# Performance work log

Hardware: AMD Instinct MI355X
Metric: run time of the kernel (lower is better)

Reference implementation:

```python
import jax, jax.numpy as jnp
import numpy as np

HEADS = 4
C = 128            # per-head out channels (hard-coded 128 in the module)
NEG_SLOPE_ATT = 0.2   # GATConv attention leaky_relu slope
NEG_SLOPE = 0.01      # F.leaky_relu default slope


def _diag_output_ids(num_groups, n):
    # ids = base_i + n*j + j for group i, agent j; base_i = i * n^2
    i = np.arange(num_groups)[:, None] * (n * n)
    j = np.arange(n)[None, :] * (n + 1)
    return jnp.asarray((i + j).reshape(-1))


def setup_inputs() -> dict:
    key = jax.random.key(0)
    ks = jax.random.split(key, 12)
    num_groups, n_agents = 12, 48
    N = num_groups * n_agents * n_agents      # 27648 nodes
    E = 442368
    F_in, edge_dim, hidden = 256, 16, 256
    s = 0.05
    return {
        "x": jax.random.normal(ks[0], (N, F_in), jnp.float32),
        "edge_index": jax.random.randint(ks[1], (2, E), 0, N, jnp.int32),
        "edge_attr": jax.random.normal(ks[2], (E, edge_dim), jnp.float32),
        "num_groups": num_groups,
        "agents_per_group": n_agents,
        "W": jax.random.normal(ks[3], (F_in, HEADS * C), jnp.float32) * s,
        "att_src": jax.random.normal(ks[4], (HEADS, C), jnp.float32) * s,
        "att_dst": jax.random.normal(ks[5], (HEADS, C), jnp.float32) * s,
        "W_edge": jax.random.normal(ks[6], (edge_dim, HEADS * C), jnp.float32) * s,
        "att_edge": jax.random.normal(ks[7], (HEADS, C), jnp.float32) * s,
        "bias_gat": jnp.zeros((HEADS * C,), jnp.float32),
        "fc_W": jax.random.normal(ks[8], (HEADS * C, hidden), jnp.float32) * s,
        "fc_b": jnp.zeros((hidden,), jnp.float32),
    }


def _gat_conv(x, src, dst, edge_attr_full, W, att_src, att_dst, W_edge, att_edge, bias):
    N = x.shape[0]
    h = (x @ W).reshape(N, HEADS, C)                       # [N,H,C]
    a_src = jnp.einsum('nhc,hc->nh', h, att_src)           # [N,H]
    a_dst = jnp.einsum('nhc,hc->nh', h, att_dst)
    he = (edge_attr_full @ W_edge).reshape(-1, HEADS, C)   # [E',H,C]
    a_edge = jnp.einsum('ehc,hc->eh', he, att_edge)
    logits = jax.nn.leaky_relu(a_src[src] + a_dst[dst] + a_edge, NEG_SLOPE_ATT)
    # segment softmax over incoming edges of each dst node
    m = jax.ops.segment_max(logits, dst, num_segments=N)   # [N,H]
    e = jnp.exp(logits - m[dst])
    s = jax.ops.segment_sum(e, dst, num_segments=N)
    alpha = e / (s[dst] + 1e-16)                           # [E',H]
    msg = h[src] * alpha[..., None]                        # [E',H,C]
    out = jax.ops.segment_sum(msg, dst, num_segments=N)    # [N,H,C]
    return out.reshape(N, HEADS * C) + bias


def reference(x, edge_index, edge_attr, num_groups, agents_per_group,
              W, att_src, att_dst, W_edge, att_edge, bias_gat, fc_W, fc_b):
    N = x.shape[0]
    # add self-loops (PyG default), self-loop edge_attr = mean fill
    loops = jnp.arange(N, dtype=edge_index.dtype)
    src = jnp.concatenate([edge_index[0], loops])
    dst = jnp.concatenate([edge_index[1], loops])
    ea = jnp.concatenate([edge_attr,
                          jnp.broadcast_to(edge_attr.mean(0), (N, edge_attr.shape[1]))])
    h = jax.nn.leaky_relu(
        _gat_conv(x, src, dst, ea, W, att_src, att_dst, W_edge, att_edge, bias_gat),
        NEG_SLOPE)
    ids = _diag_output_ids(num_groups, agents_per_group)
    # fc_output + leaky_relu then diagonal index-select (select first: same math)
    return jax.nn.leaky_relu(h[ids] @ fc_W + fc_b, NEG_SLOPE)
```

## Files before the change

kernel.cpp:

```cpp
#include <hip/hip_runtime.h>

#define NNODES 27648
#define NEDGES 442368
#define FIN    256
#define HC     512
#define NH     4
#define CDIM   128
#define NAG    48
#define NGRP   12
#define N2     2304
#define NOUT   576
#define CAP    128
#define EDIM   16
#define MPART  512
#define SCANB  (NEDGES/256)
#define ASRCB0 (SCANB + 1)


__device__ __forceinline__ float lrelu(float v, float s){ return v > 0.0f ? v : s * v; }

__device__ __forceinline__ float wsum(float v){
  #pragma unroll
  for (int off = 32; off; off >>= 1) v += __shfl_xor(v, off, 64);
  return v;
}
__device__ __forceinline__ float wmax(float v){
  #pragma unroll
  for (int off = 32; off; off >>= 1) v = fmaxf(v, __shfl_xor(v, off, 64));
  return v;
}

__global__ __launch_bounds__(256) void k_pre(
    const float* __restrict__ W, const float* __restrict__ att_src,
    const float* __restrict__ att_dst, const float* __restrict__ W_edge,
    const float* __restrict__ att_edge, const float* __restrict__ ea,
    float* __restrict__ ws_, float* __restrict__ wd_, float* __restrict__ we_,
    int* __restrict__ counts, float4* __restrict__ easum_part){
  int b = blockIdx.x;
  int tid = threadIdx.x;
  if (b < 11) {
    int g = b * 256 + tid;
    if (g < 1024) {
      int f = g >> 2, h = g & 3;
      const float4* wp = (const float4*)(W + f*HC + h*CDIM);
      const float4* ap = (const float4*)(att_src + h*CDIM);
      float s = 0.f;
      #pragma unroll 8
      for (int c4 = 0; c4 < CDIM/4; c4++){
        float4 wv = wp[c4], av = ap[c4];
        s += wv.x*av.x + wv.y*av.y + wv.z*av.z + wv.w*av.w;
      }
      ws_[g] = s;
    } else if (g < 2048) {
      int gg = g - 1024; int f = gg >> 2, h = gg & 3;
      const float4* wp = (const float4*)(W + f*HC + h*CDIM);
      const float4* ap = (const float4*)(att_dst + h*CDIM);
      float s = 0.f;
      #pragma unroll 8
      for (int c4 = 0; c4 < CDIM/4; c4++){
        float4 wv = wp[c4], av = ap[c4];
        s += wv.x*av.x + wv.y*av.y + wv.z*av.z + wv.w*av.w;
      }
      wd_[gg] = s;
    } else if (g < 2112) {
      int gg = g - 2048; int d = gg >> 2, h = gg & 3;
      const float4* wp = (const float4*)(W_edge + d*HC + h*CDIM);
      const float4* ap = (const float4*)(att_edge + h*CDIM);
      float s = 0.f;
      #pragma unroll 8
      for (int c4 = 0; c4 < CDIM/4; c4++){
        float4 wv = wp[c4], av = ap[c4];
        s += wv.x*av.x + wv.y*av.y + wv.z*av.z + wv.w*av.w;
      }
      we_[gg] = s;
    } else if (g < 2112 + NOUT) {
      counts[g - 2112] = 0;
    }
  } else {
    int pb = b - 11;
    const float4* p = (const float4*)ea;
    const int total = NEDGES * 4;
    float4 acc = make_float4(0.f, 0.f, 0.f, 0.f);
    for (int i = pb*256 + tid; i < total; i += MPART*256){
      float4 v = p[i];
      acc.x += v.x; acc.y += v.y; acc.z += v.z; acc.w += v.w;
    }
    #pragma unroll
    for (int off = 4; off <= 32; off <<= 1){
      acc.x += __shfl_xor(acc.x, off, 64);
      acc.y += __shfl_xor(acc.y, off, 64);
      acc.z += __shfl_xor(acc.z, off, 64);
      acc.w += __shfl_xor(acc.w, off, 64);
    }
    __shared__ float4 sd4[16];
    int lane = tid & 63, wave = tid >> 6;
    if (lane < 4) sd4[wave*4 + lane] = acc;
    __syncthreads();
    if (tid < 4){
      float4 t = sd4[tid];
      float4 a = sd4[4+tid], c = sd4[8+tid], d = sd4[12+tid];
      t.x += a.x + c.x + d.x; t.y += a.y + c.y + d.y;
      t.z += a.z + c.z + d.z; t.w += a.w + c.w + d.w;
      easum_part[pb*4 + tid] = t;
    }
  }
}

__global__ __launch_bounds__(256) void k_scan(const int* __restrict__ ei,
    const float* __restrict__ ea, const float* __restrict__ we_,
    const float* __restrict__ ws_, const float* __restrict__ wd_,
    const float* __restrict__ x,
    int* __restrict__ counts, int* __restrict__ slist, float* __restrict__ aed,
    const float* __restrict__ easum_part, float* __restrict__ easum,
    float* __restrict__ mal, float* __restrict__ asrc, float* __restrict__ adst){
  int tid = threadIdx.x;
  int b = blockIdx.x;
  if (b < SCANB){
    int e = b*256 + tid;
    int dst = ei[NEDGES + e];
    int r = dst % N2;
    if (r % 49) return;
    int row = (dst / N2) * NAG + r / 49;
    int pos = atomicAdd(&counts[row], 1);
    if (pos >= CAP) return;
    slist[row*CAP + pos] = ei[e];
    const float* eap = ea + (size_t)e*EDIM;
    float a0=0.f,a1=0.f,a2=0.f,a3=0.f;
    #pragma unroll
    for (int d = 0; d < EDIM; d++){
      float v = eap[d];
      a0 += v*we_[d*4+0]; a1 += v*we_[d*4+1]; a2 += v*we_[d*4+2]; a3 += v*we_[d*4+3];
    }
    float* ap = aed + (size_t)(row*CAP+pos)*4;
    ap[0]=a0; ap[1]=a1; ap[2]=a2; ap[3]=a3;
    return;
  }
  if (b == SCANB){
    int col = tid & 15, part = tid >> 4;
    float s = 0.f;
    for (int pb = 0; pb < MPART/16; pb++)
      s += easum_part[(part*(MPART/16) + pb)*16 + col];
    __shared__ float sd[256];
    __shared__ float se[16];
    sd[tid] = s;
    __syncthreads();
    if (tid < 16){
      float t = 0.f;
      #pragma unroll
      for (int i = 0; i < 16; i++) t += sd[i*16 + tid];
      easum[tid] = t;
      se[tid] = t;
    }
    __syncthreads();
    if (tid < 4){
      const float invE = 1.0f/(float)NEDGES;
      float m = 0.f;
      #pragma unroll
      for (int d = 0; d < 16; d++) m += se[d]*invE*we_[d*4+tid];
      mal[tid] = m;
    }
    return;
  }
  {
    int lane = tid & 63, wave = tid >> 6;
    int node = (b - ASRCB0)*4 + wave;
    float4 xv = *(const float4*)(x + (size_t)node*FIN + lane*4);
    float ps[4] = {0.f,0.f,0.f,0.f}, pd[4] = {0.f,0.f,0.f,0.f};
    #pragma unroll
    for (int q = 0; q < 4; q++){
      float4 wsv = *(const float4*)(ws_ + (lane*4+q)*4);
      float4 wdv = *(const float4*)(wd_ + (lane*4+q)*4);
      float xq = (q==0) ? xv.x : (q==1) ? xv.y : (q==2) ? xv.z : xv.w;
      ps[0]+=xq*wsv.x; ps[1]+=xq*wsv.y; ps[2]+=xq*wsv.z; ps[3]+=xq*wsv.w;
      pd[0]+=xq*wdv.x; pd[1]+=xq*wdv.y; pd[2]+=xq*wdv.z; pd[3]+=xq*wdv.w;
    }
    #pragma unroll
    for (int h = 0; h < 4; h++){ ps[h] = wsum(ps[h]); pd[h] = wsum(pd[h]); }
    if (lane == 0){
      *(float4*)(asrc + (size_t)node*4) = make_float4(ps[0],ps[1],ps[2],ps[3]);
      *(float4*)(adst + (size_t)node*4) = make_float4(pd[0],pd[1],pd[2],pd[3]);
    }
  }
}

__global__ __launch_bounds__(512) void k_mega(const float* __restrict__ x,
    const float* __restrict__ asrc, const float* __restrict__ adst,
    const float* __restrict__ mal,
    const int* __restrict__ counts, const int* __restrict__ slist,
    const float* __restrict__ aed,
    const float* __restrict__ W, const float* __restrict__ bias,
    const float* __restrict__ fcW, const float* __restrict__ fcb,
    float* __restrict__ out){
  __shared__ float  lg[2][(CAP+1)*4];
  __shared__ int    srcs[2][CAP+1];
  __shared__ float4 zs4[2][256];
  __shared__ float  hsf[2][512];
  __shared__ float4 scratch[2048];
  int rowA = blockIdx.x * 2;
  int tid = threadIdx.x;
  int lane = tid & 63, wave = tid >> 6;
  int rsel = wave >> 2;
  int w4 = wave & 3;

  int kA = counts[rowA];     if (kA > CAP) kA = CAP;
  int kB = counts[rowA + 1]; if (kB > CAP) kB = CAP;
  int gA = rowA / NAG,  jA = rowA - gA*NAG;
  int dstA = gA*N2 + jA*49;
  int gB = (rowA+1) / NAG, jB = (rowA+1) - gB*NAG;
  int dstB = gB*N2 + jB*49;

  {
    int r = tid >> 8;
    int i = tid & 255;
    int kk = r ? kB : kA;
    int drow = r ? dstB : dstA;
    if (i <= kk){
      int row = rowA + r;
      int src; float4 aedv;
      if (i < kk){
        src = slist[row*CAP + i];
        aedv = *(const float4*)(aed + (size_t)(row*CAP+i)*4);
      } else {
        src = drow;
        aedv = *(const float4*)mal;
      }
      float4 as = *(const float4*)(asrc + (size_t)src*4);
      float4 ad = *(const float4*)(adst + (size_t)drow*4);
      srcs[r][i] = src;
      lg[r][i*4+0] = lrelu(as.x + ad.x + aedv.x, 0.2f);
      lg[r][i*4+1] = lrelu(as.y + ad.y + aedv.y, 0.2f);
      lg[r][i*4+2] = lrelu(as.z + ad.z + aedv.z, 0.2f);
      lg[r][i*4+3] = lrelu(as.w + ad.w + aedv.w, 0.2f);
    }
  }
  __syncthreads();

  {
    int r = wave >> 2, h = wave & 3;
    int kk = r ? kB : kA;
    float m = -1e30f;
    for (int i = lane; i <= kk; i += 64) m = fmaxf(m, lg[r][i*4+h]);
    m = wmax(m);
    float s = 0.f;
    for (int i = lane; i <= kk; i += 64){
      float e = __expf(lg[r][i*4+h] - m);
      lg[r][i*4+h] = e;
      s += e;
    }
    s = wsum(s);
    float inv = 1.0f/(s + 1e-16f);
    for (int i = lane; i <= kk; i += 64) lg[r][i*4+h] *= inv;
  }
  __syncthreads();

  {
    int myK = rsel ? kB : kA;
    float acc[4][4];
    #pragma unroll
    for (int h = 0; h < 4; h++)
      #pragma unroll
      for (int c = 0; c < 4; c++) acc[h][c] = 0.f;
    for (int i = w4; i <= myK; i += 4){
      int src = srcs[rsel][i];
      float4 xv = *(const float4*)(x + (size_t)src*FIN + lane*4);
      float a0 = lg[rsel][i*4+0], a1 = lg[rsel][i*4+1];
      float a2 = lg[rsel][i*4+2], a3 = lg[rsel][i*4+3];
      acc[0][0] += a0*xv.x; acc[0][1] += a0*xv.y; acc[0][2] += a0*xv.z; acc[0][3] += a0*xv.w;
      acc[1][0] += a1*xv.x; acc[1][1] += a1*xv.y; acc[1][2] += a1*xv.z; acc[1][3] += a1*xv.w;
      acc[2][0] += a2*xv.x; acc[2][1] += a2*xv.y; acc[2][2] += a2*xv.z; acc[2][3] += a2*xv.w;
      acc[3][0] += a3*xv.x; acc[3][1] += a3*xv.y; acc[3][2] += a3*xv.z; acc[3][3] += a3*xv.w;
    }
    #pragma unroll
    for (int h = 0; h < 4; h++)
      scratch[rsel*1024 + w4*256 + h*64 + lane] =
        make_float4(acc[h][0], acc[h][1], acc[h][2], acc[h][3]);
  }
  __syncthreads();
  {
    int r = tid >> 8, s = tid & 255;
    float4 a = scratch[r*1024 + 0*256 + s], b = scratch[r*1024 + 1*256 + s];
    float4 c = scratch[r*1024 + 2*256 + s], d = scratch[r*1024 + 3*256 + s];
    zs4[r][s] = make_float4(a.x+b.x+c.x+d.x, a.y+b.y+c.y+d.y,
                            a.z+b.z+c.z+d.z, a.w+b.w+c.w+d.w);
  }
  __syncthreads();

  {
    int cg = tid & 127;
    int q  = tid >> 7;
    int h  = cg >> 5;
    const float* zA = (const float*)&zs4[0][0] + h*256 + q*64;
    const float* zB = (const float*)&zs4[1][0] + h*256 + q*64;
    const float4* Wp = (const float4*)(W + (size_t)q*64*HC) + cg;
    float4 aA = make_float4(0.f,0.f,0.f,0.f);
    float4 aB = make_float4(0.f,0.f,0.f,0.f);
    #pragma unroll 8
    for (int r = 0; r < 64; r++){
      float4 w4v = Wp[(size_t)r*(HC/4)];
      float za = zA[r], zb = zB[r];
      aA.x += za*w4v.x; aA.y += za*w4v.y; aA.z += za*w4v.z; aA.w += za*w4v.w;
      aB.x += zb*w4v.x; aB.y += zb*w4v.y; aB.z += zb*w4v.z; aB.w += zb*w4v.w;
    }
    scratch[0*512 + q*128 + cg] = aA;
    scratch[1*512 + q*128 + cg] = aB;
  }
  __syncthreads();
  if (tid < 256){
    int r = tid >> 7, cg = tid & 127;
    float4 a = scratch[r*512 + 0*128 + cg], b = scratch[r*512 + 1*128 + cg];
    float4 c = scratch[r*512 + 2*128 + cg], d = scratch[r*512 + 3*128 + cg];
    float4 bs = ((const float4*)bias)[cg];
    hsf[r][4*cg+0] = lrelu(a.x+b.x+c.x+d.x+bs.x, 0.01f);
    hsf[r][4*cg+1] = lrelu(a.y+b.y+c.y+d.y+bs.y, 0.01f);
    hsf[r][4*cg+2] = lrelu(a.z+b.z+c.z+d.z+bs.z, 0.01f);
    hsf[r][4*cg+3] = lrelu(a.w+b.w+c.w+d.w+bs.w, 0.01f);
  }
  __syncthreads();

  {
    int cg = tid & 63;
    int e  = tid >> 6;
    const float4* Fp = (const float4*)(fcW + (size_t)e*64*256) + cg;
    const float* hA = &hsf[0][0] + e*64;
    const float* hB = &hsf[1][0] + e*64;
    float4 aA = make_float4(0.f,0.f,0.f,0.f);
    float4 aB = make_float4(0.f,0.f,0.f,0.f);
    #pragma unroll 8
    for (int r = 0; r < 64; r++){
      float4 w4v = Fp[(size_t)r*64];
      float ha = hA[r], hb = hB[r];
      aA.x += ha*w4v.x; aA.y += ha*w4v.y; aA.z += ha*w4v.z; aA.w += ha*w4v.w;
      aB.x += hb*w4v.x; aB.y += hb*w4v.y; aB.z += hb*w4v.z; aB.w += hb*w4v.w;
    }
    scratch[0*512 + e*64 + cg] = aA;
    scratch[1*512 + e*64 + cg] = aB;
  }
  __syncthreads();
  if (tid < 128){
    int r = tid >> 6, cg = tid & 63;
    float4 s0 = scratch[r*512 + 0*64 + cg];
    #pragma unroll
    for (int e = 1; e < 8; e++){
      float4 t = scratch[r*512 + e*64 + cg];
      s0.x += t.x; s0.y += t.y; s0.z += t.z; s0.w += t.w;
    }
    float4 bs = ((const float4*)fcb)[cg];
    float4 o;
    o.x = lrelu(s0.x+bs.x, 0.01f);
    o.y = lrelu(s0.y+bs.y, 0.01f);
    o.z = lrelu(s0.z+bs.z, 0.01f);
    o.w = lrelu(s0.w+bs.w, 0.01f);
    *(float4*)(out + (size_t)(rowA + r)*256 + 4*cg) = o;
  }
}

extern "C" void kernel_launch(void* const* d_in, const int* in_sizes, int n_in,
                              void* d_out, int out_size, void* d_ws, size_t ws_size,
                              hipStream_t stream) {
  const float* x        = (const float*)d_in[0];
  const int*   ei       = (const int*)  d_in[1];
  const float* ea       = (const float*)d_in[2];
  const float* W        = (const float*)d_in[5];
  const float* att_src  = (const float*)d_in[6];
  const float* att_dst  = (const float*)d_in[7];
  const float* W_edge   = (const float*)d_in[8];
  const float* att_edge = (const float*)d_in[9];
  const float* bias     = (const float*)d_in[10];
  const float* fcW      = (const float*)d_in[11];
  const float* fcb      = (const float*)d_in[12];
  float* out = (float*)d_out;

  float* w = (float*)d_ws;
  float*  ws_       = w;
  float*  wd_       = w + 1024;
  float*  we_       = w + 2048;
  float*  easum     = w + 2112;
  int*    counts    = (int*)(w + 2128);
  float*  easum_p   = w + 2704;
  int*    slist     = (int*)(w + 10896);
  float*  aed       = w + 84624;
  float*  asrc      = w + 379536;
  float*  adst      = w + 490128;
  float*  mal       = w + 600720;

  k_pre<<<11 + MPART, 256, 0, stream>>>(W, att_src, att_dst, W_edge, att_edge, ea,
                                        ws_, wd_, we_, counts, (float4*)easum_p);
  k_scan<<<ASRCB0 + NNODES/4, 256, 0, stream>>>(ei, ea, we_, ws_, wd_, x,
                                                counts, slist, aed,
                                                easum_p, easum, mal, asrc, adst);
  k_mega<<<NOUT/2, 512, 0, stream>>>(x, asrc, adst, mal, counts, slist, aed,
                                     W, bias, fcW, fcb, out);
}
```

Before: 153.7 us.

## Process four output rows per block in fused GAT kernel to reuse weight loads

The fused aggregation/projection kernel now handles four diagonal output rows per block instead of two, halving the grid. Each W and fc_W element loaded from memory feeds four accumulators instead of two, cutting weight traffic per output row. The trade-off is fewer blocks (144 vs 288) on a large GPU, so parallelism and latency hiding drop, and the neighbor-gather phase has only two waves per row.

```diff
diff --git a/kernel.cpp b/kernel.cpp
--- a/kernel.cpp
+++ b/kernel.cpp
@@ -191,41 +191,38 @@
     const float* __restrict__ W, const float* __restrict__ bias,
     const float* __restrict__ fcW, const float* __restrict__ fcb,
     float* __restrict__ out){
-  __shared__ float  lg[2][(CAP+1)*4];
-  __shared__ int    srcs[2][CAP+1];
-  __shared__ float4 zs4[2][256];
-  __shared__ float  hsf[2][512];
+  __shared__ float  lg[4][(CAP+1)*4];
+  __shared__ int    srcs[4][CAP+1];
+  __shared__ float4 zs4[4][256];
+  __shared__ float  hsf[4][512];
   __shared__ float4 scratch[2048];
-  int rowA = blockIdx.x * 2;
+  int rowBase = blockIdx.x * 4;
   int tid = threadIdx.x;
   int lane = tid & 63, wave = tid >> 6;
-  int rsel = wave >> 2;
-  int w4 = wave & 3;
-
-  int kA = counts[rowA];     if (kA > CAP) kA = CAP;
-  int kB = counts[rowA + 1]; if (kB > CAP) kB = CAP;
-  int gA = rowA / NAG,  jA = rowA - gA*NAG;
-  int dstA = gA*N2 + jA*49;
-  int gB = (rowA+1) / NAG, jB = (rowA+1) - gB*NAG;
-  int dstB = gB*N2 + jB*49;
-
-  {
-    int r = tid >> 8;
-    int i = tid & 255;
-    int kk = r ? kB : kA;
-    int drow = r ? dstB : dstA;
-    if (i <= kk){
-      int row = rowA + r;
+
+  int kk[4], dsts[4];
+  #pragma unroll
+  for (int r = 0; r < 4; r++){
+    int row = rowBase + r;
+    int c = counts[row]; kk[r] = c > CAP ? CAP : c;
+    int g = row / NAG, j = row - g*NAG;
+    dsts[r] = g*N2 + j*49;
+  }
+
+  for (int idx = tid; idx < 4*(CAP+1); idx += 512){
+    int r = idx / (CAP+1), i = idx - r*(CAP+1);
+    if (i <= kk[r]){
+      int row = rowBase + r;
       int src; float4 aedv;
-      if (i < kk){
+      if (i < kk[r]){
         src = slist[row*CAP + i];
         aedv = *(const float4*)(aed + (size_t)(row*CAP+i)*4);
       } else {
-        src = drow;
+        src = dsts[r];
         aedv = *(const float4*)mal;
       }
       float4 as = *(const float4*)(asrc + (size_t)src*4);
-      float4 ad = *(const float4*)(adst + (size_t)drow*4);
+      float4 ad = *(const float4*)(adst + (size_t)dsts[r]*4);
       srcs[r][i] = src;
       lg[r][i*4+0] = lrelu(as.x + ad.x + aedv.x, 0.2f);
       lg[r][i*4+1] = lrelu(as.y + ad.y + aedv.y, 0.2f);
@@ -235,36 +232,37 @@
   }
   __syncthreads();
 
-  {
-    int r = wave >> 2, h = wave & 3;
-    int kk = r ? kB : kA;
+  for (int t = wave; t < 16; t += 8){
+    int r = t >> 2, h = t & 3;
+    int k2 = kk[r];
     float m = -1e30f;
-    for (int i = lane; i <= kk; i += 64) m = fmaxf(m, lg[r][i*4+h]);
+    for (int i = lane; i <= k2; i += 64) m = fmaxf(m, lg[r][i*4+h]);
     m = wmax(m);
     float s = 0.f;
-    for (int i = lane; i <= kk; i += 64){
+    for (int i = lane; i <= k2; i += 64){
       float e = __expf(lg[r][i*4+h] - m);
       lg[r][i*4+h] = e;
       s += e;
     }
     s = wsum(s);
     float inv = 1.0f/(s + 1e-16f);
-    for (int i = lane; i <= kk; i += 64) lg[r][i*4+h] *= inv;
-  }
-  __syncthreads();
-
-  {
-    int myK = rsel ? kB : kA;
+    for (int i = lane; i <= k2; i += 64) lg[r][i*4+h] *= inv;
+  }
+  __syncthreads();
+
+  {
+    int r = wave >> 1, w2 = wave & 1;
+    int myK = kk[r];
     float acc[4][4];
     #pragma unroll
     for (int h = 0; h < 4; h++)
       #pragma unroll
       for (int c = 0; c < 4; c++) acc[h][c] = 0.f;
-    for (int i = w4; i <= myK; i += 4){
-      int src = srcs[rsel][i];
+    for (int i = w2; i <= myK; i += 2){
+      int src = srcs[r][i];
       float4 xv = *(const float4*)(x + (size_t)src*FIN + lane*4);
-      float a0 = lg[rsel][i*4+0], a1 = lg[rsel][i*4+1];
-      float a2 = lg[rsel][i*4+2], a3 = lg[rsel][i*4+3];
+      float a0 = lg[r][i*4+0], a1 = lg[r][i*4+1];
+      float a2 = lg[r][i*4+2], a3 = lg[r][i*4+3];
       acc[0][0] += a0*xv.x; acc[0][1] += a0*xv.y; acc[0][2] += a0*xv.z; acc[0][3] += a0*xv.w;
       acc[1][0] += a1*xv.x; acc[1][1] += a1*xv.y; acc[1][2] += a1*xv.z; acc[1][3] += a1*xv.w;
       acc[2][0] += a2*xv.x; acc[2][1] += a2*xv.y; acc[2][2] += a2*xv.z; acc[2][3] += a2*xv.w;
@@ -272,16 +270,14 @@
     }
     #pragma unroll
     for (int h = 0; h < 4; h++)
-      scratch[rsel*1024 + w4*256 + h*64 + lane] =
+      scratch[r*512 + w2*256 + h*64 + lane] =
         make_float4(acc[h][0], acc[h][1], acc[h][2], acc[h][3]);
   }
   __syncthreads();
-  {
-    int r = tid >> 8, s = tid & 255;
-    float4 a = scratch[r*1024 + 0*256 + s], b = scratch[r*1024 + 1*256 + s];
-    float4 c = scratch[r*1024 + 2*256 + s], d = scratch[r*1024 + 3*256 + s];
-    zs4[r][s] = make_float4(a.x+b.x+c.x+d.x, a.y+b.y+c.y+d.y,
-                            a.z+b.z+c.z+d.z, a.w+b.w+c.w+d.w);
+  for (int f = tid; f < 1024; f += 512){
+    int r = f >> 8, s = f & 255;
+    float4 a = scratch[r*512 + s], b = scratch[r*512 + 256 + s];
+    zs4[r][s] = make_float4(a.x+b.x, a.y+b.y, a.z+b.z, a.w+b.w);
   }
   __syncthreads();
 
@@ -289,23 +285,28 @@
     int cg = tid & 127;
     int q  = tid >> 7;
     int h  = cg >> 5;
-    const float* zA = (const float*)&zs4[0][0] + h*256 + q*64;
-    const float* zB = (const float*)&zs4[1][0] + h*256 + q*64;
+    const float* z0 = (const float*)&zs4[0][0] + h*256 + q*64;
     const float4* Wp = (const float4*)(W + (size_t)q*64*HC) + cg;
     float4 aA = make_float4(0.f,0.f,0.f,0.f);
     float4 aB = make_float4(0.f,0.f,0.f,0.f);
+    float4 aC = make_float4(0.f,0.f,0.f,0.f);
+    float4 aD = make_float4(0.f,0.f,0.f,0.f);
     #pragma unroll 8
     for (int r = 0; r < 64; r++){
       float4 w4v = Wp[(size_t)r*(HC/4)];
-      float za = zA[r], zb = zB[r];
+      float za = z0[r], zb = z0[1024+r], zc = z0[2048+r], zd = z0[3072+r];
       aA.x += za*w4v.x; aA.y += za*w4v.y; aA.z += za*w4v.z; aA.w += za*w4v.w;
       aB.x += zb*w4v.x; aB.y += zb*w4v.y; aB.z += zb*w4v.z; aB.w += zb*w4v.w;
+      aC.x += zc*w4v.x; aC.y += zc*w4v.y; aC.z += zc*w4v.z; aC.w += zc*w4v.w;
+      aD.x += zd*w4v.x; aD.y += zd*w4v.y; aD.z += zd*w4v.z; aD.w += zd*w4v.w;
     }
     scratch[0*512 + q*128 + cg] = aA;
     scratch[1*512 + q*128 + cg] = aB;
-  }
-  __syncthreads();
-  if (tid < 256){
+    scratch[2*512 + q*128 + cg] = aC;
+    scratch[3*512 + q*128 + cg] = aD;
+  }
+  __syncthreads();
+  {
     int r = tid >> 7, cg = tid & 127;
     float4 a = scratch[r*512 + 0*128 + cg], b = scratch[r*512 + 1*128 + cg];
     float4 c = scratch[r*512 + 2*128 + cg], d = scratch[r*512 + 3*128 + cg];
@@ -321,24 +322,29 @@
     int cg = tid & 63;
     int e  = tid >> 6;
     const float4* Fp = (const float4*)(fcW + (size_t)e*64*256) + cg;
-    const float* hA = &hsf[0][0] + e*64;
-    const float* hB = &hsf[1][0] + e*64;
+    const float* h0 = &hsf[0][0] + e*64;
     float4 aA = make_float4(0.f,0.f,0.f,0.f);
     float4 aB = make_float4(0.f,0.f,0.f,0.f);
+    float4 aC = make_float4(0.f,0.f,0.f,0.f);
+    float4 aD = make_float4(0.f,0.f,0.f,0.f);
     #pragma unroll 8
     for (int r = 0; r < 64; r++){
       float4 w4v = Fp[(size_t)r*64];
-      float ha = hA[r], hb = hB[r];
+      float ha = h0[r], hb = h0[512+r], hc = h0[1024+r], hd = h0[1536+r];
       aA.x += ha*w4v.x; aA.y += ha*w4v.y; aA.z += ha*w4v.z; aA.w += ha*w4v.w;
       aB.x += hb*w4v.x; aB.y += hb*w4v.y; aB.z += hb*w4v.z; aB.w += hb*w4v.w;
+      aC.x += hc*w4v.x; aC.y += hc*w4v.y; aC.z += hc*w4v.z; aC.w += hc*w4v.w;
+      aD.x += hd*w4v.x; aD.y += hd*w4v.y; aD.z += hd*w4v.z; aD.w += hd*w4v.w;
     }
     scratch[0*512 + e*64 + cg] = aA;
     scratch[1*512 + e*64 + cg] = aB;
-  }
-  __syncthreads();
-  if (tid < 128){
+    scratch[2*512 + e*64 + cg] = aC;
+    scratch[3*512 + e*64 + cg] = aD;
+  }
+  __syncthreads();
+  if (tid < 256){
     int r = tid >> 6, cg = tid & 63;
-    float4 s0 = scratch[r*512 + 0*64 + cg];
+    float4 s0 = scratch[r*512 + cg];
     #pragma unroll
     for (int e = 1; e < 8; e++){
       float4 t = scratch[r*512 + e*64 + cg];
@@ -350,7 +356,7 @@
     o.y = lrelu(s0.y+bs.y, 0.01f);
     o.z = lrelu(s0.z+bs.z, 0.01f);
     o.w = lrelu(s0.w+bs.w, 0.01f);
-    *(float4*)(out + (size_t)(rowA + r)*256 + 4*cg) = o;
+    *(float4*)(out + (size_t)(rowBase + r)*256 + 4*cg) = o;
   }
 }
 
@@ -388,6 +394,6 @@
   k_scan<<<ASRCB0 + NNODES/4, 256, 0, stream>>>(ei, ea, we_, ws_, wd_, x,
                                                 counts, slist, aed,
                                                 easum_p, easum, mal, asrc, adst);
-  k_mega<<<NOUT/2, 512, 0, stream>>>(x, asrc, adst, mal, counts, slist, aed,
+  k_mega<<<NOUT/4, 512, 0, stream>>>(x, asrc, adst, mal, counts, slist, aed,
                                      W, bias, fcW, fcb, out);
 }
```

Measured after the change: 149.6 us. 2.6% less time.

## Split fused attention+GEMM kernel into attention and two row-tiled GEMM kernels

Applied to the files above, without the earlier changes.

Replaces the single mega kernel, which handled two output rows per block and streamed the full W and fc_W matrices for every pair, with three kernels. An attention kernel runs one row per block and writes the aggregated features z to workspace. Two GEMM kernels then process 8 rows per block split by head or column block, so each weight element loaded is reused across 8 rows instead of 2. This cuts redundant weight traffic and raises parallelism, at the cost of two extra launches and a round trip of the intermediates through global memory.

```diff
diff --git a/kernel.cpp b/kernel.cpp
--- a/kernel.cpp
+++ b/kernel.cpp
@@ -183,88 +183,67 @@
   }
 }
 
-__global__ __launch_bounds__(512) void k_mega(const float* __restrict__ x,
+__global__ __launch_bounds__(256) void k_attn(const float* __restrict__ x,
     const float* __restrict__ asrc, const float* __restrict__ adst,
     const float* __restrict__ mal,
     const int* __restrict__ counts, const int* __restrict__ slist,
-    const float* __restrict__ aed,
-    const float* __restrict__ W, const float* __restrict__ bias,
-    const float* __restrict__ fcW, const float* __restrict__ fcb,
-    float* __restrict__ out){
-  __shared__ float  lg[2][(CAP+1)*4];
-  __shared__ int    srcs[2][CAP+1];
-  __shared__ float4 zs4[2][256];
-  __shared__ float  hsf[2][512];
-  __shared__ float4 scratch[2048];
-  int rowA = blockIdx.x * 2;
+    const float* __restrict__ aed, float* __restrict__ z){
+  __shared__ float  lg[(CAP+1)*4];
+  __shared__ int    srcs[CAP+1];
+  __shared__ float4 pz[4*256];
+  int row = blockIdx.x;
   int tid = threadIdx.x;
   int lane = tid & 63, wave = tid >> 6;
-  int rsel = wave >> 2;
-  int w4 = wave & 3;
-
-  int kA = counts[rowA];     if (kA > CAP) kA = CAP;
-  int kB = counts[rowA + 1]; if (kB > CAP) kB = CAP;
-  int gA = rowA / NAG,  jA = rowA - gA*NAG;
-  int dstA = gA*N2 + jA*49;
-  int gB = (rowA+1) / NAG, jB = (rowA+1) - gB*NAG;
-  int dstB = gB*N2 + jB*49;
-
-  {
-    int r = tid >> 8;
-    int i = tid & 255;
-    int kk = r ? kB : kA;
-    int drow = r ? dstB : dstA;
-    if (i <= kk){
-      int row = rowA + r;
-      int src; float4 aedv;
-      if (i < kk){
-        src = slist[row*CAP + i];
-        aedv = *(const float4*)(aed + (size_t)(row*CAP+i)*4);
-      } else {
-        src = drow;
-        aedv = *(const float4*)mal;
-      }
-      float4 as = *(const float4*)(asrc + (size_t)src*4);
-      float4 ad = *(const float4*)(adst + (size_t)drow*4);
-      srcs[r][i] = src;
-      lg[r][i*4+0] = lrelu(as.x + ad.x + aedv.x, 0.2f);
-      lg[r][i*4+1] = lrelu(as.y + ad.y + aedv.y, 0.2f);
-      lg[r][i*4+2] = lrelu(as.z + ad.z + aedv.z, 0.2f);
-      lg[r][i*4+3] = lrelu(as.w + ad.w + aedv.w, 0.2f);
-    }
-  }
-  __syncthreads();
-
-  {
-    int r = wave >> 2, h = wave & 3;
-    int kk = r ? kB : kA;
+  int k = counts[row]; if (k > CAP) k = CAP;
+  int g = row / NAG, j = row - g*NAG;
+  int dst = g*N2 + j*49;
+
+  if (tid <= k){
+    int src; float4 aedv;
+    if (tid < k){
+      src = slist[row*CAP + tid];
+      aedv = *(const float4*)(aed + (size_t)(row*CAP+tid)*4);
+    } else {
+      src = dst;
+      aedv = *(const float4*)mal;
+    }
+    float4 as = *(const float4*)(asrc + (size_t)src*4);
+    float4 ad = *(const float4*)(adst + (size_t)dst*4);
+    srcs[tid] = src;
+    lg[tid*4+0] = lrelu(as.x + ad.x + aedv.x, 0.2f);
+    lg[tid*4+1] = lrelu(as.y + ad.y + aedv.y, 0.2f);
+    lg[tid*4+2] = lrelu(as.z + ad.z + aedv.z, 0.2f);
+    lg[tid*4+3] = lrelu(as.w + ad.w + aedv.w, 0.2f);
+  }
+  __syncthreads();
+
+  {
+    int h = wave;
     float m = -1e30f;
-    for (int i = lane; i <= kk; i += 64) m = fmaxf(m, lg[r][i*4+h]);
+    for (int i = lane; i <= k; i += 64) m = fmaxf(m, lg[i*4+h]);
     m = wmax(m);
     float s = 0.f;
-    for (int i = lane; i <= kk; i += 64){
-      float e = __expf(lg[r][i*4+h] - m);
-      lg[r][i*4+h] = e;
+    for (int i = lane; i <= k; i += 64){
+      float e = __expf(lg[i*4+h] - m);
+      lg[i*4+h] = e;
       s += e;
     }
     s = wsum(s);
     float inv = 1.0f/(s + 1e-16f);
-    for (int i = lane; i <= kk; i += 64) lg[r][i*4+h] *= inv;
-  }
-  __syncthreads();
-
-  {
-    int myK = rsel ? kB : kA;
+    for (int i = lane; i <= k; i += 64) lg[i*4+h] *= inv;
+  }
+  __syncthreads();
+
+  {
     float acc[4][4];
     #pragma unroll
     for (int h = 0; h < 4; h++)
       #pragma unroll
       for (int c = 0; c < 4; c++) acc[h][c] = 0.f;
-    for (int i = w4; i <= myK; i += 4){
-      int src = srcs[rsel][i];
+    for (int i = wave; i <= k; i += 4){
+      int src = srcs[i];
       float4 xv = *(const float4*)(x + (size_t)src*FIN + lane*4);
-      float a0 = lg[rsel][i*4+0], a1 = lg[rsel][i*4+1];
-      float a2 = lg[rsel][i*4+2], a3 = lg[rsel][i*4+3];
+      float a0 = lg[i*4+0], a1 = lg[i*4+1], a2 = lg[i*4+2], a3 = lg[i*4+3];
       acc[0][0] += a0*xv.x; acc[0][1] += a0*xv.y; acc[0][2] += a0*xv.z; acc[0][3] += a0*xv.w;
       acc[1][0] += a1*xv.x; acc[1][1] += a1*xv.y; acc[1][2] += a1*xv.z; acc[1][3] += a1*xv.w;
       acc[2][0] += a2*xv.x; acc[2][1] += a2*xv.y; acc[2][2] += a2*xv.z; acc[2][3] += a2*xv.w;
@@ -272,85 +251,129 @@
     }
     #pragma unroll
     for (int h = 0; h < 4; h++)
-      scratch[rsel*1024 + w4*256 + h*64 + lane] =
+      pz[wave*256 + h*64 + lane] =
         make_float4(acc[h][0], acc[h][1], acc[h][2], acc[h][3]);
   }
   __syncthreads();
   {
-    int r = tid >> 8, s = tid & 255;
-    float4 a = scratch[r*1024 + 0*256 + s], b = scratch[r*1024 + 1*256 + s];
-    float4 c = scratch[r*1024 + 2*256 + s], d = scratch[r*1024 + 3*256 + s];
-    zs4[r][s] = make_float4(a.x+b.x+c.x+d.x, a.y+b.y+c.y+d.y,
-                            a.z+b.z+c.z+d.z, a.w+b.w+c.w+d.w);
-  }
-  __syncthreads();
-
-  {
-    int cg = tid & 127;
-    int q  = tid >> 7;
-    int h  = cg >> 5;
-    const float* zA = (const float*)&zs4[0][0] + h*256 + q*64;
-    const float* zB = (const float*)&zs4[1][0] + h*256 + q*64;
-    const float4* Wp = (const float4*)(W + (size_t)q*64*HC) + cg;
-    float4 aA = make_float4(0.f,0.f,0.f,0.f);
-    float4 aB = make_float4(0.f,0.f,0.f,0.f);
+    float4 a = pz[tid], b = pz[256+tid], c = pz[512+tid], d = pz[768+tid];
+    ((float4*)(z + (size_t)row*1024))[tid] =
+      make_float4(a.x+b.x+c.x+d.x, a.y+b.y+c.y+d.y,
+                  a.z+b.z+c.z+d.z, a.w+b.w+c.w+d.w);
+  }
+}
+
+__global__ __launch_bounds__(256) void k_gemm1(const float* __restrict__ z,
+    const float* __restrict__ W, const float* __restrict__ bias,
+    float* __restrict__ h2){
+  __shared__ float  zt[256][8];
+  __shared__ float4 part[8][8][32];
+  int rb = blockIdx.x * 8;
+  int h  = blockIdx.y;
+  int tid = threadIdx.x;
+  for (int idx = tid; idx < 2048; idx += 256){
+    int r = idx >> 8, f = idx & 255;
+    zt[f][r] = z[(size_t)(rb+r)*1024 + h*256 + f];
+  }
+  __syncthreads();
+  {
+    int cg = tid & 31, q = tid >> 5;
+    const float4* Wp = (const float4*)(W + h*CDIM) + cg;
+    float4 acc[8];
+    #pragma unroll
+    for (int r = 0; r < 8; r++) acc[r] = make_float4(0.f,0.f,0.f,0.f);
+    int f0 = q*32;
     #pragma unroll 8
-    for (int r = 0; r < 64; r++){
-      float4 w4v = Wp[(size_t)r*(HC/4)];
-      float za = zA[r], zb = zB[r];
-      aA.x += za*w4v.x; aA.y += za*w4v.y; aA.z += za*w4v.z; aA.w += za*w4v.w;
-      aB.x += zb*w4v.x; aB.y += zb*w4v.y; aB.z += zb*w4v.z; aB.w += zb*w4v.w;
-    }
-    scratch[0*512 + q*128 + cg] = aA;
-    scratch[1*512 + q*128 + cg] = aB;
-  }
-  __syncthreads();
-  if (tid < 256){
-    int r = tid >> 7, cg = tid & 127;
-    float4 a = scratch[r*512 + 0*128 + cg], b = scratch[r*512 + 1*128 + cg];
-    float4 c = scratch[r*512 + 2*128 + cg], d = scratch[r*512 + 3*128 + cg];
-    float4 bs = ((const float4*)bias)[cg];
-    hsf[r][4*cg+0] = lrelu(a.x+b.x+c.x+d.x+bs.x, 0.01f);
-    hsf[r][4*cg+1] = lrelu(a.y+b.y+c.y+d.y+bs.y, 0.01f);
-    hsf[r][4*cg+2] = lrelu(a.z+b.z+c.z+d.z+bs.z, 0.01f);
-    hsf[r][4*cg+3] = lrelu(a.w+b.w+c.w+d.w+bs.w, 0.01f);
-  }
-  __syncthreads();
-
-  {
-    int cg = tid & 63;
-    int e  = tid >> 6;
-    const float4* Fp = (const float4*)(fcW + (size_t)e*64*256) + cg;
-    const float* hA = &hsf[0][0] + e*64;
-    const float* hB = &hsf[1][0] + e*64;
-    float4 aA = make_float4(0.f,0.f,0.f,0.f);
-    float4 aB = make_float4(0.f,0.f,0.f,0.f);
-    #pragma unroll 8
-    for (int r = 0; r < 64; r++){
-      float4 w4v = Fp[(size_t)r*64];
-      float ha = hA[r], hb = hB[r];
-      aA.x += ha*w4v.x; aA.y += ha*w4v.y; aA.z += ha*w4v.z; aA.w += ha*w4v.w;
-      aB.x += hb*w4v.x; aB.y += hb*w4v.y; aB.z += hb*w4v.z; aB.w += hb*w4v.w;
-    }
-    scratch[0*512 + e*64 + cg] = aA;
-    scratch[1*512 + e*64 + cg] = aB;
-  }
-  __syncthreads();
-  if (tid < 128){
-    int r = tid >> 6, cg = tid & 63;
-    float4 s0 = scratch[r*512 + 0*64 + cg];
-    #pragma unroll
-    for (int e = 1; e < 8; e++){
-      float4 t = scratch[r*512 + e*64 + cg];
+    for (int jf = 0; jf < 32; jf++){
+      int f = f0 + jf;
+      float4 w4 = Wp[(size_t)f*(HC/4)];
+      float4 zlo = *(const float4*)&zt[f][0];
+      float4 zhi = *(const float4*)&zt[f][4];
+      acc[0].x += zlo.x*w4.x; acc[0].y += zlo.x*w4.y; acc[0].z += zlo.x*w4.z; acc[0].w += zlo.x*w4.w;
+      acc[1].x += zlo.y*w4.x; acc[1].y += zlo.y*w4.y; acc[1].z += zlo.y*w4.z; acc[1].w += zlo.y*w4.w;
+      acc[2].x += zlo.z*w4.x; acc[2].y += zlo.z*w4.y; acc[2].z += zlo.z*w4.z; acc[2].w += zlo.z*w4.w;
+      acc[3].x += zlo.w*w4.x; acc[3].y += zlo.w*w4.y; acc[3].z += zlo.w*w4.z; acc[3].w += zlo.w*w4.w;
+      acc[4].x += zhi.x*w4.x; acc[4].y += zhi.x*w4.y; acc[4].z += zhi.x*w4.z; acc[4].w += zhi.x*w4.w;
+      acc[5].x += zhi.y*w4.x; acc[5].y += zhi.y*w4.y; acc[5].z += zhi.y*w4.z; acc[5].w += zhi.y*w4.w;
+      acc[6].x += zhi.z*w4.x; acc[6].y += zhi.z*w4.y; acc[6].z += zhi.z*w4.z; acc[6].w += zhi.z*w4.w;
+      acc[7].x += zhi.w*w4.x; acc[7].y += zhi.w*w4.y; acc[7].z += zhi.w*w4.z; acc[7].w += zhi.w*w4.w;
+    }
+    #pragma unroll
+    for (int r = 0; r < 8; r++) part[q][r][cg] = acc[r];
+  }
+  __syncthreads();
+  {
+    int r = tid >> 5, cg = tid & 31;
+    float4 s0 = part[0][r][cg];
+    #pragma unroll
+    for (int q = 1; q < 8; q++){
+      float4 t = part[q][r][cg];
       s0.x += t.x; s0.y += t.y; s0.z += t.z; s0.w += t.w;
     }
-    float4 bs = ((const float4*)fcb)[cg];
+    float4 bs = ((const float4*)bias)[h*32 + cg];
     float4 o;
     o.x = lrelu(s0.x+bs.x, 0.01f);
     o.y = lrelu(s0.y+bs.y, 0.01f);
     o.z = lrelu(s0.z+bs.z, 0.01f);
     o.w = lrelu(s0.w+bs.w, 0.01f);
-    *(float4*)(out + (size_t)(rowA + r)*256 + 4*cg) = o;
+    *(float4*)(h2 + (size_t)(rb+r)*HC + h*CDIM + 4*cg) = o;
+  }
+}
+
+__global__ __launch_bounds__(256) void k_gemm2(const float* __restrict__ h2,
+    const float* __restrict__ fcW, const float* __restrict__ fcb,
+    float* __restrict__ out){
+  __shared__ float  ht[512][8];
+  __shared__ float4 part[16][8][16];
+  int rb = blockIdx.x * 8;
+  int cb = blockIdx.y;
+  int tid = threadIdx.x;
+  for (int idx = tid; idx < 4096; idx += 256){
+    int r = idx >> 9, kf = idx & 511;
+    ht[kf][r] = h2[(size_t)(rb+r)*HC + kf];
+  }
+  __syncthreads();
+  {
+    int cg = tid & 15, q = tid >> 4;
+    const float4* Fp = (const float4*)(fcW + cb*64) + cg;
+    float4 acc[8];
+    #pragma unroll
+    for (int r = 0; r < 8; r++) acc[r] = make_float4(0.f,0.f,0.f,0.f);
+    int k0 = q*32;
+    #pragma unroll 8
+    for (int jk = 0; jk < 32; jk++){
+      int kf = k0 + jk;
+      float4 w4 = Fp[(size_t)kf*64];
+      float4 hlo = *(const float4*)&ht[kf][0];
+      float4 hhi = *(const float4*)&ht[kf][4];
+      acc[0].x += hlo.x*w4.x; acc[0].y += hlo.x*w4.y; acc[0].z += hlo.x*w4.z; acc[0].w += hlo.x*w4.w;
+      acc[1].x += hlo.y*w4.x; acc[1].y += hlo.y*w4.y; acc[1].z += hlo.y*w4.z; acc[1].w += hlo.y*w4.w;
+      acc[2].x += hlo.z*w4.x; acc[2].y += hlo.z*w4.y; acc[2].z += hlo.z*w4.z; acc[2].w += hlo.z*w4.w;
+      acc[3].x += hlo.w*w4.x; acc[3].y += hlo.w*w4.y; acc[3].z += hlo.w*w4.z; acc[3].w += hlo.w*w4.w;
+      acc[4].x += hhi.x*w4.x; acc[4].y += hhi.x*w4.y; acc[4].z += hhi.x*w4.z; acc[4].w += hhi.x*w4.w;
+      acc[5].x += hhi.y*w4.x; acc[5].y += hhi.y*w4.y; acc[5].z += hhi.y*w4.z; acc[5].w += hhi.y*w4.w;
+      acc[6].x += hhi.z*w4.x; acc[6].y += hhi.z*w4.y; acc[6].z += hhi.z*w4.z; acc[6].w += hhi.z*w4.w;
+      acc[7].x += hhi.w*w4.x; acc[7].y += hhi.w*w4.y; acc[7].z += hhi.w*w4.z; acc[7].w += hhi.w*w4.w;
+    }
+    #pragma unroll
+    for (int r = 0; r < 8; r++) part[q][r][cg] = acc[r];
+  }
+  __syncthreads();
+  if (tid < 128){
+    int r = tid >> 4, cg = tid & 15;
+    float4 s0 = part[0][r][cg];
+    #pragma unroll
+    for (int q = 1; q < 16; q++){
+      float4 t = part[q][r][cg];
+      s0.x += t.x; s0.y += t.y; s0.z += t.z; s0.w += t.w;
+    }
+    float4 bs = ((const float4*)fcb)[cb*16 + cg];
+    float4 o;
+    o.x = lrelu(s0.x+bs.x, 0.01f);
+    o.y = lrelu(s0.y+bs.y, 0.01f);
+    o.z = lrelu(s0.z+bs.z, 0.01f);
+    o.w = lrelu(s0.w+bs.w, 0.01f);
+    *(float4*)(out + (size_t)(rb+r)*256 + cb*64 + 4*cg) = o;
   }
 }
 
@@ -382,12 +405,15 @@
   float*  asrc      = w + 379536;
   float*  adst      = w + 490128;
   float*  mal       = w + 600720;
+  float*  z         = w + 600724;
+  float*  h2        = w + 1190548;
 
   k_pre<<<11 + MPART, 256, 0, stream>>>(W, att_src, att_dst, W_edge, att_edge, ea,
                                         ws_, wd_, we_, counts, (float4*)easum_p);
   k_scan<<<ASRCB0 + NNODES/4, 256, 0, stream>>>(ei, ea, we_, ws_, wd_, x,
                                                 counts, slist, aed,
                                                 easum_p, easum, mal, asrc, adst);
-  k_mega<<<NOUT/2, 512, 0, stream>>>(x, asrc, adst, mal, counts, slist, aed,
-                                     W, bias, fcW, fcb, out);
-}
+  k_attn<<<NOUT, 256, 0, stream>>>(x, asrc, adst, mal, counts, slist, aed, z);
+  k_gemm1<<<dim3(NOUT/8, 4), 256, 0, stream>>>(z, W, bias, h2);
+  k_gemm2<<<dim3(NOUT/8, 4), 256, 0, stream>>>(h2, fcW, fcb, out);
+}
```

New measurement: 150.0 us. -2.4%, faster.
